# Kernel tuning notes

Hardware: AMD Instinct MI355X
Metric: run time of the kernel (lower is better)

The kernel has to match this reference:

```python
import jax, jax.numpy as jnp
import numpy as np

D = 1024      # model dim
H = 16        # num heads
HD = D // H   # head dim = 64
B, N, M = 4, 4096, 256
EPS = 1e-12   # torch F.normalize eps


def setup_inputs() -> dict:
    key = jax.random.key(0)
    ks = jax.random.split(key, 11)
    s = 0.02  # weight init scale
    W = lambda k: jax.random.normal(k, (D, D), jnp.float32) * s
    return {
        "x": jax.random.normal(ks[0], (B, N, D), jnp.float32),
        "c": jax.random.normal(ks[1], (B, M, D), jnp.float32),
        "Wq_x": W(ks[2]), "Wk_x": W(ks[3]), "Wv_x": W(ks[4]),
        "Wq_c": W(ks[5]), "Wk_c": W(ks[6]), "Wv_c": W(ks[7]),
        "Wo_x": W(ks[8]), "Wo_c": W(ks[9]),
        "norm_const": 0.5 * jnp.ones((1, H, 1, 1), jnp.float32),
    }


def _heads(t):
    # (B, S, D) -> (B, H, S, HD)
    b, s, _ = t.shape
    return t.reshape(b, s, H, HD).transpose(0, 2, 1, 3)


def _l2norm(t):
    n = jnp.linalg.norm(t, axis=-1, keepdims=True)
    return t / jnp.maximum(n, EPS)


def reference(x, c, Wq_x, Wk_x, Wv_x, Wq_c, Wk_c, Wv_c, Wo_x, Wo_c, norm_const):
    b, n, d = x.shape
    m = c.shape[1]
    # fused QKV projections for each stream (Linear, no bias: y = t @ W^T)
    qx = _l2norm(_heads(x @ Wq_x.T))   # (B,H,N,HD), cosine-normalized
    kx = _l2norm(_heads(x @ Wk_x.T))
    vx = _heads(x @ Wv_x.T)
    qc = _l2norm(_heads(c @ Wq_c.T))   # (B,H,M,HD)
    kc = _l2norm(_heads(c @ Wk_c.T))
    vc = _heads(c @ Wv_c.T)
    # concat streams along the sequence axis
    q = jnp.concatenate([qx, qc], axis=2)   # (B,H,N+M,HD)
    k = jnp.concatenate([kx, kc], axis=2)
    v = jnp.concatenate([vx, vc], axis=2)
    n_tot = n + m
    # cosine (linear) attention, non-causal: values scaled by N^sigmoid(norm_const)
    v = v / (jnp.float32(n_tot) ** jax.nn.sigmoid(norm_const))
    kv = jnp.einsum("bhnd,bhne->bhde", k, v)         # (B,H,HD,HD)
    attn = jnp.einsum("bhnd,bhde->bhne", q, kv)      # (B,H,N+M,HD)
    # split streams, merge heads, output projections
    attn_x = attn[:, :, :n].transpose(0, 2, 1, 3).reshape(b, n, H * HD)
    attn_c = attn[:, :, n:].transpose(0, 2, 1, 3).reshape(b, m, H * HD)
    out_x = attn_x @ Wo_x.T
    out_c = attn_c @ Wo_c.T
    return out_x, out_c
```

## Files before the change

kernel.cpp:

```cpp
#include <hip/hip_runtime.h>
#include <cstdint>

typedef unsigned int u32;
typedef unsigned short u16;
typedef float fx4 __attribute__((ext_vector_type(4)));
typedef __bf16 bfx8 __attribute__((ext_vector_type(8)));

__device__ __forceinline__ u16 f2bf(float f) {
  u32 u = __builtin_bit_cast(u32, f);
  u32 r = (u + 0x7fffu + ((u >> 16) & 1u)) >> 16;
  return (u16)r;
}
__device__ __forceinline__ float bf2f(u16 v) {
  return __builtin_bit_cast(float, (u32)v << 16);
}
__device__ __forceinline__ void async_copy16(const void* g, void* l) {
  auto gp = reinterpret_cast<__attribute__((address_space(1))) void*>((uintptr_t)g);
  auto lp = reinterpret_cast<__attribute__((address_space(3))) void*>((uintptr_t)l);
  __builtin_amdgcn_global_load_lds(gp, lp, 16, 0, 0);
}

__global__ __launch_bounds__(256) void cvt_all(
    const float* __restrict__ x, const float* __restrict__ c,
    const float* __restrict__ w0, const float* __restrict__ w1,
    const float* __restrict__ w2, const float* __restrict__ w3,
    const float* __restrict__ w4, const float* __restrict__ w5,
    const float* __restrict__ w6, const float* __restrict__ w7,
    u16* __restrict__ xb, u16* __restrict__ cb, u16* __restrict__ wb) {
  const int i = blockIdx.x * 256 + threadIdx.x;
  const float* src;
  u16* dst;
  size_t off;
  if (i < 4194304) {
    src = x; dst = xb; off = (size_t)i;
  } else if (i < 4456448) {
    src = c; dst = cb; off = (size_t)(i - 4194304);
  } else {
    const int r = i - 4456448;
    const int wsel = r >> 18;
    off = (size_t)(r & 262143);
    switch (wsel) {
      case 0: src = w0; break; case 1: src = w1; break;
      case 2: src = w2; break; case 3: src = w3; break;
      case 4: src = w4; break; case 5: src = w5; break;
      case 6: src = w6; break; default: src = w7; break;
    }
    dst = wb + (size_t)wsel * 1048576;
  }
  const fx4 v = *(const fx4*)(src + off * 4);
  uint2 o;
  o.x = (u32)f2bf(v[0]) | ((u32)f2bf(v[1]) << 16);
  o.y = (u32)f2bf(v[2]) | ((u32)f2bf(v[3]) << 16);
  *(uint2*)(dst + off * 4) = o;
}

__device__ __forceinline__ void gemm_core_k1024(
    const u16* __restrict__ A, const u16* __restrict__ Bw,
    long rowBase, long colBase, u16* As, u16* Bs, fx4 (&acc)[4][4]) {
  const int t = threadIdx.x;
  const int lane = t & 63;
  const int lr = lane & 15;
  const int quad = lane >> 4;
  const int sw = lr & 7;
  const int w = t >> 6;
  const int m0 = (w & 1) * 64;
  const int n0 = (w >> 1) * 64;
  const int f0 = t * 8;

  for (int k0 = 0; k0 < 1024; k0 += 64) {
#pragma unroll
    for (int r = 0; r < 4; ++r) {
      const int f = f0 + r * 2048;
      const int row = f >> 6;
      const int gst = (f >> 3) & 7;
      const int col = ((gst ^ (row & 7)) << 3);
      async_copy16(A + (rowBase + row) * 1024 + (k0 + col), &As[f]);
      async_copy16(Bw + (colBase + row) * 1024 + (k0 + col), &Bs[f]);
    }
    __syncthreads();
#pragma unroll
    for (int ks = 0; ks < 2; ++ks) {
      bfx8 af[4], bfr[4];
      const int g = ((ks * 4 + quad) ^ sw) << 3;
#pragma unroll
      for (int i = 0; i < 4; ++i)
        af[i] = *(const bfx8*)&As[(m0 + i * 16 + lr) * 64 + g];
#pragma unroll
      for (int i = 0; i < 4; ++i)
        bfr[i] = *(const bfx8*)&Bs[(n0 + i * 16 + lr) * 64 + g];
#pragma unroll
      for (int mi = 0; mi < 4; ++mi)
#pragma unroll
        for (int ni = 0; ni < 4; ++ni)
          acc[mi][ni] =
              __builtin_amdgcn_mfma_f32_16x16x32_bf16(af[mi], bfr[ni], acc[mi][ni], 0, 0, 0);
    }
    __syncthreads();
  }
}

__global__ __launch_bounds__(256) void proj_fused(
    const u16* __restrict__ Xb, const u16* __restrict__ Cb, const u16* __restrict__ Wb,
    u16* __restrict__ Qx, u16* __restrict__ Qc,
    u16* __restrict__ Kt, u16* __restrict__ Vt,
    const float* __restrict__ nc) {
  __shared__ __align__(16) u16 LDSbuf[2 * 128 * 64];
  u16* As = LDSbuf;
  u16* Bs = LDSbuf + 8192;
  const bool isC = blockIdx.y >= 128;
  const u16* A = isC ? Cb : Xb;
  const u16* Bw = Wb + (isC ? 3145728 : 0);
  const long rowBase = (long)(isC ? blockIdx.y - 128 : blockIdx.y) * 128;
  const long colBase = (long)blockIdx.x * 128;

  fx4 acc[4][4] = {};
  gemm_core_k1024(A, Bw, rowBase, colBase, As, Bs, acc);

  const int t = threadIdx.x;
  const int lane = t & 63;
  const int lr = lane & 15;
  const int quad = lane >> 4;
  const int w = t >> 6;
  const int m0 = (w & 1) * 64;
  const int n0 = (w >> 1) * 64;

  const long col0 = colBase + n0;
  const int col64 = (int)(col0 >> 6);
  const int sel = col64 >> 4;
  const int h = col64 & 15;
  const int lcolBase = (int)(col0 & 1023);

  if (sel == 0) {
    u16* dst = isC ? Qc : Qx;
#pragma unroll
    for (int mi = 0; mi < 4; ++mi) {
      float ss[4] = {0.f, 0.f, 0.f, 0.f};
#pragma unroll
      for (int ni = 0; ni < 4; ++ni)
#pragma unroll
        for (int r = 0; r < 4; ++r) ss[r] += acc[mi][ni][r] * acc[mi][ni][r];
#pragma unroll
      for (int off = 1; off < 16; off <<= 1)
#pragma unroll
        for (int r = 0; r < 4; ++r) ss[r] += __shfl_xor(ss[r], off, 64);
      float sc[4];
#pragma unroll
      for (int r = 0; r < 4; ++r) sc[r] = 1.f / fmaxf(sqrtf(ss[r]), 1e-12f);
#pragma unroll
      for (int ni = 0; ni < 4; ++ni) {
        const long col = lcolBase + ni * 16 + lr;
#pragma unroll
        for (int r = 0; r < 4; ++r) {
          const long row = rowBase + m0 + mi * 16 + quad * 4 + r;
          dst[row * 1024 + col] = f2bf(acc[mi][ni][r] * sc[r]);
        }
      }
    }
  } else {
    u16* LT = LDSbuf + w * 4096;
    u16* T = (sel == 1) ? Kt : Vt;
    const long R0 = rowBase + m0;
    int b, nglob0;
    if (!isC) { b = (int)(R0 >> 12); nglob0 = (int)(R0 & 4095); }
    else      { b = (int)(R0 >> 8);  nglob0 = 4096 + (int)(R0 & 255); }
    u16* Tw = T + (size_t)(b * 16 + h) * 64 * 4352;
    const float vs = __expf(-8.3783908f / (1.f + __expf(-nc[h])));

#pragma unroll
    for (int mi = 0; mi < 4; ++mi) {
      float sc[4];
      if (sel == 1) {
        float ss[4] = {0.f, 0.f, 0.f, 0.f};
#pragma unroll
        for (int ni = 0; ni < 4; ++ni)
#pragma unroll
          for (int r = 0; r < 4; ++r) ss[r] += acc[mi][ni][r] * acc[mi][ni][r];
#pragma unroll
        for (int off = 1; off < 16; off <<= 1)
#pragma unroll
          for (int r = 0; r < 4; ++r) ss[r] += __shfl_xor(ss[r], off, 64);
#pragma unroll
        for (int r = 0; r < 4; ++r) sc[r] = 1.f / fmaxf(sqrtf(ss[r]), 1e-12f);
      } else {
#pragma unroll
        for (int r = 0; r < 4; ++r) sc[r] = vs;
      }
      const int g = 2 * mi + (quad >> 1);
      const int sub = (quad & 1) * 4;
#pragma unroll
      for (int ni = 0; ni < 4; ++ni) {
        const int d = ni * 16 + lr;
        uint2 o;
        o.x = (u32)f2bf(acc[mi][ni][0] * sc[0]) | ((u32)f2bf(acc[mi][ni][1] * sc[1]) << 16);
        o.y = (u32)f2bf(acc[mi][ni][2] * sc[2]) | ((u32)f2bf(acc[mi][ni][3] * sc[3]) << 16);
        *(uint2*)&LT[d * 64 + ((g ^ (d & 7)) << 3) + sub] = o;
      }
    }
    __syncthreads();
    const int d = lane;
    u16* drow = Tw + (size_t)d * 4352 + nglob0;
#pragma unroll
    for (int j = 0; j < 8; ++j) {
      const uint4 qv = *(const uint4*)&LT[d * 64 + ((j ^ (d & 7)) << 3)];
      *(uint4*)&drow[j * 8] = qv;
    }
  }
}

__global__ __launch_bounds__(256) void kv_mfma(
    const u16* __restrict__ Kt, const u16* __restrict__ Vt, float* __restrict__ kvb) {
  __shared__ __align__(16) u16 TT[4][2][4096];
  const int bh = blockIdx.x;
  const int t = threadIdx.x;
  const int w = t >> 6;
  const int lane = t & 63;
  const int lr = lane & 15;
  const int quad = lane >> 4;
  const u16* Ksrc = Kt + (size_t)bh * 64 * 4352;
  const u16* Vsrc = Vt + (size_t)bh * 64 * 4352;
  const int row8 = lane >> 3;
  const int gst = lane & 7;
  fx4 acc[4][4] = {};

  for (int s = 0; s < 17; ++s) {
    const int kbase = w * 1088 + s * 64;
#pragma unroll
    for (int i = 0; i < 8; ++i) {
      const int row = i * 8 + row8;
      const int col = ((gst ^ (row & 7)) << 3);
      const size_t go = (size_t)row * 4352 + kbase + col;
      async_copy16(Ksrc + go, &TT[w][0][i * 512 + lane * 8]);
      async_copy16(Vsrc + go, &TT[w][1][i * 512 + lane * 8]);
    }
    __syncthreads();
#pragma unroll
    for (int ks = 0; ks < 2; ++ks) {
      bfx8 af[4], bfr[4];
      const int g = ((ks * 4 + quad) ^ (lr & 7)) << 3;
#pragma unroll
      for (int i = 0; i < 4; ++i) af[i] = *(const bfx8*)&TT[w][0][(i * 16 + lr) * 64 + g];
#pragma unroll
      for (int i = 0; i < 4; ++i) bfr[i] = *(const bfx8*)&TT[w][1][(i * 16 + lr) * 64 + g];
#pragma unroll
      for (int mi = 0; mi < 4; ++mi)
#pragma unroll
        for (int ni = 0; ni < 4; ++ni)
          acc[mi][ni] =
              __builtin_amdgcn_mfma_f32_16x16x32_bf16(af[mi], bfr[ni], acc[mi][ni], 0, 0, 0);
    }
    __syncthreads();
  }
  float* red = (float*)&TT[0][0][0];
  float* my = red + w * 4096;
#pragma unroll
  for (int mi = 0; mi < 4; ++mi)
#pragma unroll
    for (int ni = 0; ni < 4; ++ni) {
      const int e = ni * 16 + lr;
      const int dg = mi * 4 + quad;
      *(fx4*)&my[e * 64 + ((dg ^ (e & 15)) << 2)] = acc[mi][ni];
    }
  __syncthreads();
  float* outp = kvb + (size_t)bh * 4096;
#pragma unroll
  for (int j = 0; j < 4; ++j) {
    const int L = t * 16 + j * 4;
    const int e = L >> 6;
    const int dg = (L >> 2) & 15;
    const int addr = e * 64 + ((dg ^ (e & 15)) << 2);
    fx4 sv = *(const fx4*)&red[addr];
    sv += *(const fx4*)&red[4096 + addr];
    sv += *(const fx4*)&red[8192 + addr];
    sv += *(const fx4*)&red[12288 + addr];
    *(fx4*)&outp[L] = sv;
  }
}

__global__ __launch_bounds__(256) void weff_build(
    const u16* __restrict__ WoX, const u16* __restrict__ WoC,
    const float* __restrict__ kvb, u16* __restrict__ WeffX, u16* __restrict__ WeffC) {
  const int ot = blockIdx.x;
  const int bh = blockIdx.y;
  const int b = bh >> 4, h = bh & 15;
  const u16* Wo = blockIdx.z ? WoC : WoX;
  u16* outp = (blockIdx.z ? WeffC : WeffX) + (size_t)b * 1048576;

  __shared__ __align__(16) float kvT[64 * 64];
  __shared__ __align__(16) float WoT[64 * 64];
  const int t = threadIdx.x;
#pragma unroll
  for (int j = 0; j < 4; ++j) {
    const int idx = (t + 256 * j) * 4;
    *(fx4*)&kvT[idx] = *(const fx4*)&kvb[(size_t)bh * 4096 + idx];
  }
#pragma unroll
  for (int j = 0; j < 2; ++j) {
    const int u = t + 256 * j;
    const int row = u >> 3;
    const int e0 = (u & 7) * 8;
    const uint4 q = *(const uint4*)&Wo[(size_t)(ot * 64 + row) * 1024 + h * 64 + e0];
    WoT[(e0 + 0) * 64 + row] = bf2f((u16)(q.x & 0xffff));
    WoT[(e0 + 1) * 64 + row] = bf2f((u16)(q.x >> 16));
    WoT[(e0 + 2) * 64 + row] = bf2f((u16)(q.y & 0xffff));
    WoT[(e0 + 3) * 64 + row] = bf2f((u16)(q.y >> 16));
    WoT[(e0 + 4) * 64 + row] = bf2f((u16)(q.z & 0xffff));
    WoT[(e0 + 5) * 64 + row] = bf2f((u16)(q.z >> 16));
    WoT[(e0 + 6) * 64 + row] = bf2f((u16)(q.w & 0xffff));
    WoT[(e0 + 7) * 64 + row] = bf2f((u16)(q.w >> 16));
  }
  __syncthreads();
  const int ob = (t >> 4) * 4;
  const int db = (t & 15) * 4;
  float acc[4][4] = {};
#pragma unroll 4
  for (int e = 0; e < 64; ++e) {
    const fx4 wv = *(const fx4*)&WoT[e * 64 + ob];
    const fx4 kvv = *(const fx4*)&kvT[e * 64 + db];
#pragma unroll
    for (int i = 0; i < 4; ++i)
#pragma unroll
      for (int j = 0; j < 4; ++j)
        acc[i][j] += wv[i] * kvv[j];
  }
#pragma unroll
  for (int i = 0; i < 4; ++i)
#pragma unroll
    for (int j = 0; j < 4; ++j)
      outp[(size_t)(ot * 64 + ob + i) * 1024 + h * 64 + db + j] = f2bf(acc[i][j]);
}

__global__ __launch_bounds__(256) void out_fused(
    const u16* __restrict__ Qx, const u16* __restrict__ Qc,
    const u16* __restrict__ Wex, const u16* __restrict__ Wec,
    float* __restrict__ out) {
  __shared__ __align__(16) u16 As[128 * 64];
  __shared__ __align__(16) u16 Bs[128 * 64];
  const int yt = blockIdx.y;
  const int b = yt / 34;
  const int local = yt - b * 34;
  const bool isC = local >= 32;
  const u16* A;
  const u16* Bw;
  float* C;
  long rowBase;
  if (!isC) {
    A = Qx + (size_t)b * 4194304;
    Bw = Wex + (size_t)b * 1048576;
    C = out + (size_t)b * 4194304;
    rowBase = (long)local * 128;
  } else {
    A = Qc + (size_t)b * 262144;
    Bw = Wec + (size_t)b * 1048576;
    C = out + 16777216 + (size_t)b * 262144;
    rowBase = (long)(local - 32) * 128;
  }
  const long colBase = (long)blockIdx.x * 128;

  fx4 acc[4][4] = {};
  gemm_core_k1024(A, Bw, rowBase, colBase, As, Bs, acc);

  const int t = threadIdx.x;
  const int lane = t & 63;
  const int lr = lane & 15;
  const int quad = lane >> 4;
  const int w = t >> 6;
  const int m0 = (w & 1) * 64;
  const int n0 = (w >> 1) * 64;
#pragma unroll
  for (int mi = 0; mi < 4; ++mi)
#pragma unroll
    for (int ni = 0; ni < 4; ++ni) {
      const long col = colBase + n0 + ni * 16 + lr;
#pragma unroll
      for (int r = 0; r < 4; ++r) {
        const long row = rowBase + m0 + mi * 16 + quad * 4 + r;
        C[row * 1024 + col] = acc[mi][ni][r];
      }
    }
}

extern "C" void kernel_launch(void* const* d_in, const int* in_sizes, int n_in,
                              void* d_out, int out_size, void* d_ws, size_t ws_size,
                              hipStream_t stream) {
  (void)in_sizes; (void)n_in; (void)out_size; (void)ws_size;
  const float* x = (const float*)d_in[0];
  const float* c = (const float*)d_in[1];
  const float* nc = (const float*)d_in[10];
  float* out = (float*)d_out;
  char* ws = (char*)d_ws;

  u16* Xb = (u16*)(ws + 0);
  u16* Cb = (u16*)(ws + 33554432);
  u16* Wb = (u16*)(ws + 35651584);
  u16* Qx = (u16*)(ws + 52428800);
  u16* Qc = (u16*)(ws + 85983232);
  u16* Kt = (u16*)(ws + 88080384);
  u16* Vt = (u16*)(ws + 123731968);
  float* kvb = (float*)(ws + 159383552);
  u16* Weffx = (u16*)(ws + 160432128);
  u16* Weffc = (u16*)(ws + 168820736);

  cvt_all<<<25600, 256, 0, stream>>>(
      x, c, (const float*)d_in[2], (const float*)d_in[3], (const float*)d_in[4],
      (const float*)d_in[5], (const float*)d_in[6], (const float*)d_in[7],
      (const float*)d_in[8], (const float*)d_in[9], Xb, Cb, Wb);

  proj_fused<<<dim3(24, 136), 256, 0, stream>>>(Xb, Cb, Wb, Qx, Qc, Kt, Vt, nc);
  kv_mfma<<<64, 256, 0, stream>>>(Kt, Vt, kvb);
  weff_build<<<dim3(16, 64, 2), 256, 0, stream>>>(Wb + 6 * 1048576, Wb + 7 * 1048576,
                                                  kvb, Weffx, Weffc);
  out_fused<<<dim3(8, 136), 256, 0, stream>>>(Qx, Qc, Weffx, Weffc, out);
}
```

Measured before the change: 431.0 us.

## Use 256x256 GEMM tiles with a 4-stage async LDS pipeline

Replaces the 128x128 single-buffered GEMM core with a 256x256 tile computed by 512 threads (8 waves). It uses a 4-slot ring of K=32 stages in LDS, prefetching 3 stages ahead with waitcnt-controlled barriers and raising wave priority around the MFMA blocks. Both the projection and output kernels move to this core with 128KB of dynamic LDS, and their epilogues are adapted to the 8x4 accumulator layout. The aim is to hide global-load latency and raise data reuse per tile. In exchange it allows only one block per CU and launches fewer, larger blocks, which hurts tail balance.

Result: faster. 419.3 us (-2.7%).

```diff
diff --git a/kernel.cpp b/kernel.cpp
--- a/kernel.cpp
+++ b/kernel.cpp
@@ -54,77 +54,123 @@
   *(uint2*)(dst + off * 4) = o;
 }
 
-__device__ __forceinline__ void gemm_core_k1024(
+__device__ __forceinline__ void gemm256_core(
     const u16* __restrict__ A, const u16* __restrict__ Bw,
-    long rowBase, long colBase, u16* As, u16* Bs, fx4 (&acc)[4][4]) {
-  const int t = threadIdx.x;
-  const int lane = t & 63;
-  const int lr = lane & 15;
-  const int quad = lane >> 4;
-  const int sw = lr & 7;
-  const int w = t >> 6;
-  const int m0 = (w & 1) * 64;
-  const int n0 = (w >> 1) * 64;
-  const int f0 = t * 8;
-
-  for (int k0 = 0; k0 < 1024; k0 += 64) {
-#pragma unroll
-    for (int r = 0; r < 4; ++r) {
-      const int f = f0 + r * 2048;
-      const int row = f >> 6;
-      const int gst = (f >> 3) & 7;
-      const int col = ((gst ^ (row & 7)) << 3);
-      async_copy16(A + (rowBase + row) * 1024 + (k0 + col), &As[f]);
-      async_copy16(Bw + (colBase + row) * 1024 + (k0 + col), &Bs[f]);
-    }
-    __syncthreads();
-#pragma unroll
-    for (int ks = 0; ks < 2; ++ks) {
-      bfx8 af[4], bfr[4];
-      const int g = ((ks * 4 + quad) ^ sw) << 3;
-#pragma unroll
-      for (int i = 0; i < 4; ++i)
-        af[i] = *(const bfx8*)&As[(m0 + i * 16 + lr) * 64 + g];
-#pragma unroll
-      for (int i = 0; i < 4; ++i)
-        bfr[i] = *(const bfx8*)&Bs[(n0 + i * 16 + lr) * 64 + g];
-#pragma unroll
-      for (int mi = 0; mi < 4; ++mi)
-#pragma unroll
-        for (int ni = 0; ni < 4; ++ni)
-          acc[mi][ni] =
-              __builtin_amdgcn_mfma_f32_16x16x32_bf16(af[mi], bfr[ni], acc[mi][ni], 0, 0, 0);
-    }
-    __syncthreads();
-  }
-}
-
-__global__ __launch_bounds__(256) void proj_fused(
-    const u16* __restrict__ Xb, const u16* __restrict__ Cb, const u16* __restrict__ Wb,
-    u16* __restrict__ Qx, u16* __restrict__ Qc,
-    u16* __restrict__ Kt, u16* __restrict__ Vt,
-    const float* __restrict__ nc) {
-  __shared__ __align__(16) u16 LDSbuf[2 * 128 * 64];
-  u16* As = LDSbuf;
-  u16* Bs = LDSbuf + 8192;
-  const bool isC = blockIdx.y >= 128;
-  const u16* A = isC ? Cb : Xb;
-  const u16* Bw = Wb + (isC ? 3145728 : 0);
-  const long rowBase = (long)(isC ? blockIdx.y - 128 : blockIdx.y) * 128;
-  const long colBase = (long)blockIdx.x * 128;
-
-  fx4 acc[4][4] = {};
-  gemm_core_k1024(A, Bw, rowBase, colBase, As, Bs, acc);
-
+    long rowBase, long colBase, u16* lds, fx4 (&acc)[8][4]) {
   const int t = threadIdx.x;
   const int lane = t & 63;
   const int lr = lane & 15;
   const int quad = lane >> 4;
   const int w = t >> 6;
-  const int m0 = (w & 1) * 64;
-  const int n0 = (w >> 1) * 64;
-
-  const long col0 = colBase + n0;
+  const int wr = w >> 2;
+  const int wc = w & 3;
+
+  const int fA0 = t * 8;
+  int dA[2];
+  const u16* gA[2];
+  const u16* gB[2];
+#pragma unroll
+  for (int r = 0; r < 2; ++r) {
+    const int f = fA0 + r * 4096;
+    const int row = f >> 5;
+    const int gst = (f >> 3) & 3;
+    const int scol = ((gst ^ (row & 3)) << 3);
+    dA[r] = f;
+    gA[r] = A + (size_t)(rowBase + row) * 1024 + scol;
+    gB[r] = Bw + (size_t)(colBase + row) * 1024 + scol;
+  }
+  const int swk = (quad ^ (lr & 3)) << 3;
+  const int abase = (wr * 128 + lr) * 32 + swk;
+  const int bbase = 8192 + (wc * 64 + lr) * 32 + swk;
+
+#pragma unroll
+  for (int pt = 0; pt < 3; ++pt) {
+    u16* slot = lds + pt * 16384;
+#pragma unroll
+    for (int r = 0; r < 2; ++r) {
+      async_copy16(gA[r] + pt * 32, slot + dA[r]);
+      async_copy16(gB[r] + pt * 32, slot + 8192 + dA[r]);
+    }
+  }
+  asm volatile("s_waitcnt vmcnt(8)" ::: "memory");
+  __builtin_amdgcn_s_barrier();
+  __builtin_amdgcn_sched_barrier(0);
+
+  for (int tt = 0; tt < 32; ++tt) {
+    u16* slot = lds + (tt & 3) * 16384;
+    bfx8 bfr[4], af[4];
+#pragma unroll
+    for (int i = 0; i < 4; ++i) bfr[i] = *(const bfx8*)(slot + bbase + i * 512);
+#pragma unroll
+    for (int i = 0; i < 4; ++i) af[i] = *(const bfx8*)(slot + abase + i * 512);
+    if (tt < 29) {
+      u16* nslot = lds + ((tt + 3) & 3) * 16384;
+      const int ko = (tt + 3) * 32;
+#pragma unroll
+      for (int r = 0; r < 2; ++r) {
+        async_copy16(gA[r] + ko, nslot + dA[r]);
+        async_copy16(gB[r] + ko, nslot + 8192 + dA[r]);
+      }
+    }
+    __builtin_amdgcn_s_setprio(1);
+#pragma unroll
+    for (int mi = 0; mi < 4; ++mi)
+#pragma unroll
+      for (int ni = 0; ni < 4; ++ni)
+        acc[mi][ni] =
+            __builtin_amdgcn_mfma_f32_16x16x32_bf16(af[mi], bfr[ni], acc[mi][ni], 0, 0, 0);
+    __builtin_amdgcn_s_setprio(0);
+#pragma unroll
+    for (int i = 0; i < 4; ++i)
+      af[i] = *(const bfx8*)(slot + abase + 2048 + i * 512);
+    __builtin_amdgcn_s_setprio(1);
+#pragma unroll
+    for (int mi = 0; mi < 4; ++mi)
+#pragma unroll
+      for (int ni = 0; ni < 4; ++ni)
+        acc[4 + mi][ni] =
+            __builtin_amdgcn_mfma_f32_16x16x32_bf16(af[mi], bfr[ni], acc[4 + mi][ni], 0, 0, 0);
+    __builtin_amdgcn_s_setprio(0);
+    __builtin_amdgcn_sched_barrier(0);
+    if (tt < 29) {
+      asm volatile("s_waitcnt vmcnt(8) lgkmcnt(0)" ::: "memory");
+      __builtin_amdgcn_s_barrier();
+    } else if (tt == 29) {
+      asm volatile("s_waitcnt vmcnt(4) lgkmcnt(0)" ::: "memory");
+      __builtin_amdgcn_s_barrier();
+    } else if (tt == 30) {
+      asm volatile("s_waitcnt vmcnt(0) lgkmcnt(0)" ::: "memory");
+      __builtin_amdgcn_s_barrier();
+    }
+    __builtin_amdgcn_sched_barrier(0);
+  }
+}
+
+__global__ __launch_bounds__(512, 2) void proj_fused(
+    const u16* __restrict__ Xb, const u16* __restrict__ Cb, const u16* __restrict__ Wb,
+    u16* __restrict__ Qx, u16* __restrict__ Qc,
+    u16* __restrict__ Kt, u16* __restrict__ Vt,
+    const float* __restrict__ nc) {
+  extern __shared__ __align__(16) u16 lds[];
+  const bool isC = blockIdx.y >= 64;
+  const u16* A = isC ? Cb : Xb;
+  const u16* Bw = Wb + (isC ? 3145728 : 0);
+  const long rowBase = (long)(isC ? blockIdx.y - 64 : blockIdx.y) * 256;
+  const long colBase = (long)blockIdx.x * 256;
+
+  fx4 acc[8][4] = {};
+  gemm256_core(A, Bw, rowBase, colBase, lds, acc);
+
+  const int t = threadIdx.x;
+  const int lane = t & 63;
+  const int lr = lane & 15;
+  const int quad = lane >> 4;
+  const int w = t >> 6;
+  const int wr = w >> 2;
+  const int wc = w & 3;
+  const long wRowBase = rowBase + wr * 128;
+
+  const long col0 = colBase + wc * 64;
   const int col64 = (int)(col0 >> 6);
   const int sel = col64 >> 4;
   const int h = col64 & 15;
@@ -133,7 +179,7 @@
   if (sel == 0) {
     u16* dst = isC ? Qc : Qx;
 #pragma unroll
-    for (int mi = 0; mi < 4; ++mi) {
+    for (int mi = 0; mi < 8; ++mi) {
       float ss[4] = {0.f, 0.f, 0.f, 0.f};
 #pragma unroll
       for (int ni = 0; ni < 4; ++ni)
@@ -151,23 +197,23 @@
         const long col = lcolBase + ni * 16 + lr;
 #pragma unroll
         for (int r = 0; r < 4; ++r) {
-          const long row = rowBase + m0 + mi * 16 + quad * 4 + r;
+          const long row = wRowBase + mi * 16 + quad * 4 + r;
           dst[row * 1024 + col] = f2bf(acc[mi][ni][r] * sc[r]);
         }
       }
     }
   } else {
-    u16* LT = LDSbuf + w * 4096;
+    __syncthreads();
+    u16* LT = lds + w * 8192;
     u16* T = (sel == 1) ? Kt : Vt;
-    const long R0 = rowBase + m0;
     int b, nglob0;
-    if (!isC) { b = (int)(R0 >> 12); nglob0 = (int)(R0 & 4095); }
-    else      { b = (int)(R0 >> 8);  nglob0 = 4096 + (int)(R0 & 255); }
+    if (!isC) { b = (int)(wRowBase >> 12); nglob0 = (int)(wRowBase & 4095); }
+    else      { b = (int)(wRowBase >> 8);  nglob0 = 4096 + (int)(wRowBase & 255); }
     u16* Tw = T + (size_t)(b * 16 + h) * 64 * 4352;
     const float vs = __expf(-8.3783908f / (1.f + __expf(-nc[h])));
 
 #pragma unroll
-    for (int mi = 0; mi < 4; ++mi) {
+    for (int mi = 0; mi < 8; ++mi) {
       float sc[4];
       if (sel == 1) {
         float ss[4] = {0.f, 0.f, 0.f, 0.f};
@@ -185,7 +231,7 @@
 #pragma unroll
         for (int r = 0; r < 4; ++r) sc[r] = vs;
       }
-      const int g = 2 * mi + (quad >> 1);
+      const int g = mi * 2 + (quad >> 1);
       const int sub = (quad & 1) * 4;
 #pragma unroll
       for (int ni = 0; ni < 4; ++ni) {
@@ -193,15 +239,15 @@
         uint2 o;
         o.x = (u32)f2bf(acc[mi][ni][0] * sc[0]) | ((u32)f2bf(acc[mi][ni][1] * sc[1]) << 16);
         o.y = (u32)f2bf(acc[mi][ni][2] * sc[2]) | ((u32)f2bf(acc[mi][ni][3] * sc[3]) << 16);
-        *(uint2*)&LT[d * 64 + ((g ^ (d & 7)) << 3) + sub] = o;
+        *(uint2*)&LT[d * 128 + ((g ^ (d & 15)) << 3) + sub] = o;
       }
     }
     __syncthreads();
     const int d = lane;
     u16* drow = Tw + (size_t)d * 4352 + nglob0;
 #pragma unroll
-    for (int j = 0; j < 8; ++j) {
-      const uint4 qv = *(const uint4*)&LT[d * 64 + ((j ^ (d & 7)) << 3)];
+    for (int j = 0; j < 16; ++j) {
+      const uint4 qv = *(const uint4*)&LT[d * 128 + ((j ^ (d & 15)) << 3)];
       *(uint4*)&drow[j * 8] = qv;
     }
   }
@@ -329,16 +375,15 @@
       outp[(size_t)(ot * 64 + ob + i) * 1024 + h * 64 + db + j] = f2bf(acc[i][j]);
 }
 
-__global__ __launch_bounds__(256) void out_fused(
+__global__ __launch_bounds__(512, 2) void out_fused(
     const u16* __restrict__ Qx, const u16* __restrict__ Qc,
     const u16* __restrict__ Wex, const u16* __restrict__ Wec,
     float* __restrict__ out) {
-  __shared__ __align__(16) u16 As[128 * 64];
-  __shared__ __align__(16) u16 Bs[128 * 64];
+  extern __shared__ __align__(16) u16 lds[];
   const int yt = blockIdx.y;
-  const int b = yt / 34;
-  const int local = yt - b * 34;
-  const bool isC = local >= 32;
+  const int b = yt / 17;
+  const int l = yt - b * 17;
+  const bool isC = (l == 16);
   const u16* A;
   const u16* Bw;
   float* C;
@@ -347,33 +392,33 @@
     A = Qx + (size_t)b * 4194304;
     Bw = Wex + (size_t)b * 1048576;
     C = out + (size_t)b * 4194304;
-    rowBase = (long)local * 128;
+    rowBase = (long)l * 256;
   } else {
     A = Qc + (size_t)b * 262144;
     Bw = Wec + (size_t)b * 1048576;
     C = out + 16777216 + (size_t)b * 262144;
-    rowBase = (long)(local - 32) * 128;
-  }
-  const long colBase = (long)blockIdx.x * 128;
-
-  fx4 acc[4][4] = {};
-  gemm_core_k1024(A, Bw, rowBase, colBase, As, Bs, acc);
+    rowBase = 0;
+  }
+  const long colBase = (long)blockIdx.x * 256;
+
+  fx4 acc[8][4] = {};
+  gemm256_core(A, Bw, rowBase, colBase, lds, acc);
 
   const int t = threadIdx.x;
   const int lane = t & 63;
   const int lr = lane & 15;
   const int quad = lane >> 4;
   const int w = t >> 6;
-  const int m0 = (w & 1) * 64;
-  const int n0 = (w >> 1) * 64;
-#pragma unroll
-  for (int mi = 0; mi < 4; ++mi)
+  const int wr = w >> 2;
+  const int wc = w & 3;
+#pragma unroll
+  for (int mi = 0; mi < 8; ++mi)
 #pragma unroll
     for (int ni = 0; ni < 4; ++ni) {
-      const long col = colBase + n0 + ni * 16 + lr;
+      const long col = colBase + wc * 64 + ni * 16 + lr;
 #pragma unroll
       for (int r = 0; r < 4; ++r) {
-        const long row = rowBase + m0 + mi * 16 + quad * 4 + r;
+        const long row = rowBase + wr * 128 + mi * 16 + quad * 4 + r;
         C[row * 1024 + col] = acc[mi][ni][r];
       }
     }
@@ -388,6 +433,15 @@
   const float* nc = (const float*)d_in[10];
   float* out = (float*)d_out;
   char* ws = (char*)d_ws;
+
+  static bool attr_done = false;
+  if (!attr_done) {
+    hipFuncSetAttribute((const void*)proj_fused,
+                        hipFuncAttributeMaxDynamicSharedMemorySize, 131072);
+    hipFuncSetAttribute((const void*)out_fused,
+                        hipFuncAttributeMaxDynamicSharedMemorySize, 131072);
+    attr_done = true;
+  }
 
   u16* Xb = (u16*)(ws + 0);
   u16* Cb = (u16*)(ws + 33554432);
@@ -405,9 +459,9 @@
       (const float*)d_in[5], (const float*)d_in[6], (const float*)d_in[7],
       (const float*)d_in[8], (const float*)d_in[9], Xb, Cb, Wb);
 
-  proj_fused<<<dim3(24, 136), 256, 0, stream>>>(Xb, Cb, Wb, Qx, Qc, Kt, Vt, nc);
+  proj_fused<<<dim3(12, 68), 512, 131072, stream>>>(Xb, Cb, Wb, Qx, Qc, Kt, Vt, nc);
   kv_mfma<<<64, 256, 0, stream>>>(Kt, Vt, kvb);
   weff_build<<<dim3(16, 64, 2), 256, 0, stream>>>(Wb + 6 * 1048576, Wb + 7 * 1048576,
                                                   kvb, Weffx, Weffc);
-  out_fused<<<dim3(8, 136), 256, 0, stream>>>(Qx, Qc, Weffx, Weffc, out);
-}
+  out_fused<<<dim3(4, 68), 512, 131072, stream>>>(Qx, Qc, Weffx, Weffc, out);
+}
```
